# Optimization experiments

Measured on AMD Instinct MI355X. Metric: run time of the kernel, lower is better.

## Reference

```python
import jax, jax.numpy as jnp
import numpy as np

# LIF parameters (norse defaults, matching lif_params in init_kwargs)
TAU_MEM_INV = 100.0
TAU_SYN_INV = 200.0
V_LEAK = 0.0
V_TH = 1.0
V_RESET = 0.0
DT = 0.001
POOL = (2, 2)

B, C, H, W = 16, 64, 256, 256


def setup_inputs() -> dict:
    key = jax.random.key(0)
    input_signal = jax.random.normal(key, (B, C, H, W), dtype=jnp.float32)
    membrane = jnp.zeros((B, C, H, W), dtype=jnp.float32)
    synaptic = jnp.zeros((B, C, H, W), dtype=jnp.float32)
    return {"input_signal": input_signal, "membrane": membrane, "synaptic": synaptic}


def reference(input_signal, membrane, synaptic):
    # Single-timestep LIF update per pixel (Euler integration):
    #   i' = i + dt * tau_syn_inv * (-i) + input
    #   v' = v + dt * tau_mem_inv * ((v_leak - v) + i')
    #   spike = v' >= v_th
    i_new = synaptic * (1.0 - DT * TAU_SYN_INV) + input_signal
    v_new = membrane + DT * TAU_MEM_INV * ((V_LEAK - membrane) + i_new)
    spikes = jnp.where(v_new >= V_TH, 1.0, 0.0).astype(input_signal.dtype)
    # Max-pool the spike map over non-overlapping POOL windows.
    ph, pw = POOL
    b, c, h, w = spikes.shape
    pooled = spikes.reshape(b, c, h // ph, ph, w // pw, pw).max(axis=(3, 5))
    return pooled  # [B, C, H//ph, W//pw]
```

## Files before the change

### kernel.cpp

```cpp
#include <hip/hip_runtime.h>


constexpr int B = 16, C = 64, H = 256, W = 256;
constexpr int W4  = W / 4;
constexpr int OW2 = (W / 2) / 2;
constexpr int OROWS = B * C * (H / 2);
constexpr int NTHREADS = (OROWS / 2) * W4;

__device__ __forceinline__ float lif_v(float m, float s, float x) {
    return fmaf(0.9f, m, 0.1f * fmaf(0.8f, s, x));
}

__device__ __forceinline__ float2 pool2(const float4& Ma, const float4& Sa, const float4& Xa,
                                        const float4& Mb, const float4& Sb, const float4& Xb) {
    float a0 = lif_v(Ma.x, Sa.x, Xa.x), a1 = lif_v(Ma.y, Sa.y, Xa.y);
    float a2 = lif_v(Ma.z, Sa.z, Xa.z), a3 = lif_v(Ma.w, Sa.w, Xa.w);
    float b0 = lif_v(Mb.x, Sb.x, Xb.x), b1 = lif_v(Mb.y, Sb.y, Xb.y);
    float b2 = lif_v(Mb.z, Sb.z, Xb.z), b3 = lif_v(Mb.w, Sb.w, Xb.w);
    float w0 = fmaxf(fmaxf(a0, a1), fmaxf(b0, b1));
    float w1 = fmaxf(fmaxf(a2, a3), fmaxf(b2, b3));
    float2 o;
    o.x = (w0 >= 1.0f) ? 1.0f : 0.0f;
    o.y = (w1 >= 1.0f) ? 1.0f : 0.0f;
    return o;
}

__global__ __launch_bounds__(256) void lif_pool_kernel(
    const float4* __restrict__ x,
    const float4* __restrict__ m,
    const float4* __restrict__ s,
    float2* __restrict__ out)
{
    int t = blockIdx.x * blockDim.x + threadIdx.x;
    int g  = t & 63;
    int rp = t >> 6;

    int ib = rp * 4 * W4 + g;

    float4 X0 = x[ib], X1 = x[ib + W4], X2 = x[ib + 2 * W4], X3 = x[ib + 3 * W4];
    float4 M0 = m[ib], M1 = m[ib + W4], M2 = m[ib + 2 * W4], M3 = m[ib + 3 * W4];
    float4 S0 = s[ib], S1 = s[ib + W4], S2 = s[ib + 2 * W4], S3 = s[ib + 3 * W4];

    float2 o0 = pool2(M0, S0, X0, M1, S1, X1);
    float2 o1 = pool2(M2, S2, X2, M3, S3, X3);

    int ob = rp * 2 * OW2 + g;
    out[ob] = o0;
    out[ob + OW2] = o1;
}

extern "C" void kernel_launch(void* const* d_in, const int* in_sizes, int n_in,
                              void* d_out, int out_size, void* d_ws, size_t ws_size,
                              hipStream_t stream) {
    const float4* x = (const float4*)d_in[0];
    const float4* m = (const float4*)d_in[1];
    const float4* s = (const float4*)d_in[2];
    float2* out = (float2*)d_out;

    constexpr int BLOCK = 256;
    constexpr int GRID = NTHREADS / BLOCK;
    lif_pool_kernel<<<GRID, BLOCK, 0, stream>>>(x, m, s, out);
}
```

Before: 668.2 us.

## Switch to grid-stride loop with software-prefetched next iteration loads

Replaces the one-shot grid (each thread handling four input rows) with a fixed 2048-block grid-stride loop where each thread handles one output row pair per iteration. The loads for the next iteration are issued before the current one is computed, overlapping memory latency with compute. This cuts block-launch overhead but lowers per-thread memory parallelism within an iteration and depends on enough waves being resident to saturate bandwidth.

```diff
diff --git a/kernel.cpp b/kernel.cpp
--- a/kernel.cpp
+++ b/kernel.cpp
@@ -3,26 +3,18 @@
 
 constexpr int B = 16, C = 64, H = 256, W = 256;
 constexpr int W4  = W / 4;
-constexpr int OW2 = (W / 2) / 2;
-constexpr int OROWS = B * C * (H / 2);
-constexpr int NTHREADS = (OROWS / 2) * W4;
+constexpr int TOTAL = (B * C * H / 2) * W4;
+constexpr int BLOCK = 256;
+constexpr int GRID = 2048;
+constexpr int STRIDE = BLOCK * GRID;
+constexpr int ITERS = TOTAL / STRIDE;
 
 __device__ __forceinline__ float lif_v(float m, float s, float x) {
     return fmaf(0.9f, m, 0.1f * fmaf(0.8f, s, x));
 }
 
-__device__ __forceinline__ float2 pool2(const float4& Ma, const float4& Sa, const float4& Xa,
-                                        const float4& Mb, const float4& Sb, const float4& Xb) {
-    float a0 = lif_v(Ma.x, Sa.x, Xa.x), a1 = lif_v(Ma.y, Sa.y, Xa.y);
-    float a2 = lif_v(Ma.z, Sa.z, Xa.z), a3 = lif_v(Ma.w, Sa.w, Xa.w);
-    float b0 = lif_v(Mb.x, Sb.x, Xb.x), b1 = lif_v(Mb.y, Sb.y, Xb.y);
-    float b2 = lif_v(Mb.z, Sb.z, Xb.z), b3 = lif_v(Mb.w, Sb.w, Xb.w);
-    float w0 = fmaxf(fmaxf(a0, a1), fmaxf(b0, b1));
-    float w1 = fmaxf(fmaxf(a2, a3), fmaxf(b2, b3));
-    float2 o;
-    o.x = (w0 >= 1.0f) ? 1.0f : 0.0f;
-    o.y = (w1 >= 1.0f) ? 1.0f : 0.0f;
-    return o;
+__device__ __forceinline__ int in_base(int t) {
+    return ((t >> 6) * 2) * W4 + (t & 63);
 }
 
 __global__ __launch_bounds__(256) void lif_pool_kernel(
@@ -31,22 +23,38 @@
     const float4* __restrict__ s,
     float2* __restrict__ out)
 {
-    int t = blockIdx.x * blockDim.x + threadIdx.x;
-    int g  = t & 63;
-    int rp = t >> 6;
+    int t = blockIdx.x * BLOCK + threadIdx.x;
 
-    int ib = rp * 4 * W4 + g;
+    int ia = in_base(t);
+    float4 X0 = x[ia], X1 = x[ia + W4];
+    float4 M0 = m[ia], M1 = m[ia + W4];
+    float4 S0 = s[ia], S1 = s[ia + W4];
 
-    float4 X0 = x[ib], X1 = x[ib + W4], X2 = x[ib + 2 * W4], X3 = x[ib + 3 * W4];
-    float4 M0 = m[ib], M1 = m[ib + W4], M2 = m[ib + 2 * W4], M3 = m[ib + 3 * W4];
-    float4 S0 = s[ib], S1 = s[ib + W4], S2 = s[ib + 2 * W4], S3 = s[ib + 3 * W4];
+#pragma unroll
+    for (int i = 0; i < ITERS; ++i) {
+        float4 nX0, nX1, nM0, nM1, nS0, nS1;
+        int tn = t + STRIDE;
+        if (i + 1 < ITERS) {
+            int ib = in_base(tn);
+            nX0 = x[ib]; nX1 = x[ib + W4];
+            nM0 = m[ib]; nM1 = m[ib + W4];
+            nS0 = s[ib]; nS1 = s[ib + W4];
+        }
 
-    float2 o0 = pool2(M0, S0, X0, M1, S1, X1);
-    float2 o1 = pool2(M2, S2, X2, M3, S3, X3);
+        float a0 = lif_v(M0.x, S0.x, X0.x), a1 = lif_v(M0.y, S0.y, X0.y);
+        float a2 = lif_v(M0.z, S0.z, X0.z), a3 = lif_v(M0.w, S0.w, X0.w);
+        float b0 = lif_v(M1.x, S1.x, X1.x), b1 = lif_v(M1.y, S1.y, X1.y);
+        float b2 = lif_v(M1.z, S1.z, X1.z), b3 = lif_v(M1.w, S1.w, X1.w);
+        float w0 = fmaxf(fmaxf(a0, a1), fmaxf(b0, b1));
+        float w1 = fmaxf(fmaxf(a2, a3), fmaxf(b2, b3));
+        float2 o;
+        o.x = (w0 >= 1.0f) ? 1.0f : 0.0f;
+        o.y = (w1 >= 1.0f) ? 1.0f : 0.0f;
+        out[t] = o;
 
-    int ob = rp * 2 * OW2 + g;
-    out[ob] = o0;
-    out[ob + OW2] = o1;
+        X0 = nX0; X1 = nX1; M0 = nM0; M1 = nM1; S0 = nS0; S1 = nS1;
+        t = tn;
+    }
 }
 
 extern "C" void kernel_launch(void* const* d_in, const int* in_sizes, int n_in,
@@ -57,7 +65,5 @@
     const float4* s = (const float4*)d_in[2];
     float2* out = (float2*)d_out;
 
-    constexpr int BLOCK = 256;
-    constexpr int GRID = NTHREADS / BLOCK;
     lif_pool_kernel<<<GRID, BLOCK, 0, stream>>>(x, m, s, out);
 }
```

New measurement: 680.0 us. About the same (+1.8%).
